# Performance work log

Hardware: AMD Instinct MI355X
Metric: run time of the kernel (lower is better)

The kernel has to match this reference:

```python
import jax, jax.numpy as jnp
import numpy as np

N_TOPICS = 1024
TOPIC_DIM = 128
HIDDEN = 512
N_HEADS = 8
HEAD_DIM = HIDDEN // N_HEADS
N_LAYERS = 2
ALPHA = 0.2
TIME_DECAY = 0.1
BATCH = 8


def setup_inputs() -> dict:
    key = jax.random.key(0)
    ks = jax.random.split(key, 16)
    inp = {
        'topic_ids': jax.random.randint(ks[0], (BATCH,), 0, N_TOPICS, dtype=jnp.int32),
        'adj_matrix': jax.random.randint(ks[1], (BATCH, N_TOPICS, N_TOPICS), 0, 2, dtype=jnp.int32),
        'time_matrix': jax.random.uniform(ks[2], (BATCH, N_TOPICS, N_TOPICS), dtype=jnp.float32),
        'attractiveness': jax.random.normal(ks[3], (BATCH,), dtype=jnp.float32),
        # parameters (torch Linear convention: W [out,in], y = x@W.T + b)
        'topic_embedding': jax.random.normal(ks[4], (N_TOPICS, TOPIC_DIM), dtype=jnp.float32) * 0.1,
        'struct_W': jax.random.normal(ks[5], (HIDDEN, TOPIC_DIM), dtype=jnp.float32) * 0.05,
        'struct_b': jnp.zeros((HIDDEN,), dtype=jnp.float32),
        'attract_W': jax.random.normal(ks[6], (HIDDEN, 1), dtype=jnp.float32) * 0.05,
        'attract_b': jnp.zeros((HIDDEN,), dtype=jnp.float32),
        'gat_W': jax.random.normal(ks[7], (N_LAYERS, N_HEADS, HIDDEN, HEAD_DIM), dtype=jnp.float32) * 0.05,
        'gat_a': jax.random.normal(ks[8], (N_LAYERS, N_HEADS, 2 * HEAD_DIM, 1), dtype=jnp.float32) * 0.05,
        'fc1_W': jax.random.normal(ks[9], (HIDDEN, HIDDEN), dtype=jnp.float32) * 0.05,
        'fc1_b': jnp.zeros((HIDDEN,), dtype=jnp.float32),
        'fc2_W': jax.random.normal(ks[10], (1, HIDDEN), dtype=jnp.float32) * 0.05,
        'fc2_b': jnp.zeros((1,), dtype=jnp.float32),
    }
    return inp


def _gat_layer(node, adj, time_w, W, a):
    # node: [B,N,F], adj: [B,N,N] (0/1), time_w: [B,N,N]
    # W: [H,F,hd], a: [H,2*hd,1]
    h = jnp.einsum('bni,hio->bhno', node, W)  # [B,H,N,hd]
    # Additive attention: a = [a_src; a_dst] so e_ij = LeakyReLU(h_i.a_src + h_j.a_dst)
    a_src = a[:, :HEAD_DIM, 0]   # [H,hd]
    a_dst = a[:, HEAD_DIM:, 0]   # [H,hd]
    e_src = jnp.einsum('bhnd,hd->bhn', h, a_src)  # [B,H,N]
    e_dst = jnp.einsum('bhnd,hd->bhn', h, a_dst)  # [B,H,N]
    e = e_src[:, :, :, None] + e_dst[:, :, None, :]  # [B,H,N,N]
    e = jax.nn.leaky_relu(e, negative_slope=ALPHA)
    e = e * time_w[:, None, :, :]
    e = jnp.where(adj[:, None, :, :] == 0, -jnp.inf, e)
    attn = jax.nn.softmax(e, axis=-1)
    out = jnp.einsum('bhij,bhjd->bhid', attn, h)  # [B,H,N,hd]
    out = out.transpose(0, 2, 1, 3).reshape(node.shape[0], node.shape[1], -1)
    return jax.nn.elu(out)


def reference(topic_ids, adj_matrix, time_matrix, attractiveness,
              topic_embedding, struct_W, struct_b, attract_W, attract_b,
              gat_W, gat_a, fc1_W, fc1_b, fc2_W, fc2_b):
    # structural features for all topics -> hidden
    struct = topic_embedding @ struct_W.T + struct_b          # [N,hidden]
    attract = attractiveness[:, None] @ attract_W.T + attract_b  # [B,hidden]
    node = jnp.broadcast_to(struct[None], (BATCH, N_TOPICS, HIDDEN))
    # weighted co-occurrence time (eq.17)
    time_w = jnp.exp(-TIME_DECAY * (time_matrix.max() - time_matrix))  # [B,N,N]
    for l in range(N_LAYERS):
        node = _gat_layer(node, adj_matrix, time_w, gat_W[l], gat_a[l])
    # gather per-sample topic node feature
    topic_feat = jnp.take_along_axis(node, topic_ids[:, None, None].astype(jnp.int32), axis=1)[:, 0]  # [B,hidden]
    combined = topic_feat + attract
    hidden = jax.nn.relu(combined @ fc1_W.T + fc1_b)
    pred = hidden @ fc2_W.T + fc2_b  # [B,1]
    return pred
```

## Files before the change

kernel.cpp:

```cpp
#include <hip/hip_runtime.h>

#define NT 1024
#define TD 128
#define HID 512
#define NH 8
#define HD 64
#define NB 8

typedef unsigned short us;
typedef _Float16 h16;
typedef h16 half8 __attribute__((ext_vector_type(8)));
typedef h16 h16x2 __attribute__((ext_vector_type(2)));
typedef float f32x4 __attribute__((ext_vector_type(4)));

#define LOG2E 1.44269504f

extern "C" __device__ _Float16 __ocml_exp2_f16(_Float16);

__device__ __forceinline__ us f2h(float x) { return __builtin_bit_cast(us, (h16)x); }
__device__ __forceinline__ float h2f(us s) { return (float)__builtin_bit_cast(h16, s); }
__device__ __forceinline__ unsigned int pkh2(float a, float b) {
    auto v = __builtin_amdgcn_cvt_pkrtz(a, b);
    return __builtin_bit_cast(unsigned int, v);
}

__global__ __launch_bounds__(256) void kprep(const float* __restrict__ tm, float* __restrict__ part,
                                             const float* __restrict__ emb, const float* __restrict__ sW,
                                             const float* __restrict__ sb, us* __restrict__ node0b,
                                             const float* __restrict__ gW, us* __restrict__ Wt,
                                             const float* __restrict__ fc2b, float* __restrict__ out) {
    __shared__ __align__(16) float smf[8768];
    int bx = blockIdx.x, t = threadIdx.x;
    if (bx < 1024) {
        const float4* tm4 = (const float4*)tm;
        size_t base = (size_t)bx * 256 + t;
        float m = -1e30f;
        #pragma unroll
        for (int k = 0; k < 8; k++) {
            float4 v = tm4[base + (size_t)k * 262144];
            m = fmaxf(m, fmaxf(fmaxf(v.x, v.y), fmaxf(v.z, v.w)));
        }
        smf[t] = m; __syncthreads();
        for (int s = 128; s > 0; s >>= 1) { if (t < s) smf[t] = fmaxf(smf[t], smf[t + s]); __syncthreads(); }
        if (t == 0) part[bx] = smf[0];
    } else if (bx < 1152) {
        int g = bx - 1024; int iblk = g & 15, oseg = g >> 4;
        us* As = (us*)smf;
        us* Bs = (us*)smf + 64 * 136;
        const float4* esrc = (const float4*)(emb + (size_t)iblk * 64 * TD);
        const float4* wsrc = (const float4*)(sW + (size_t)oseg * 64 * TD);
        #pragma unroll
        for (int rep = 0; rep < 8; rep++) {
            int f = rep * 256 + t;
            int row = f >> 5, c4 = f & 31;
            float4 av = esrc[f];
            float4 bv = wsrc[f];
            uint2 pa, pb;
            pa.x = pkh2(av.x, av.y); pa.y = pkh2(av.z, av.w);
            pb.x = pkh2(bv.x, bv.y); pb.y = pkh2(bv.z, bv.w);
            *(uint2*)&As[row * 136 + c4 * 4] = pa;
            *(uint2*)&Bs[row * 136 + c4 * 4] = pb;
        }
        __syncthreads();
        int l = t & 63, w = t >> 6, m = l & 15, q = l >> 4;
        f32x4 acc[4];
        #pragma unroll
        for (int ot = 0; ot < 4; ot++) acc[ot] = (f32x4){0.f, 0.f, 0.f, 0.f};
        #pragma unroll
        for (int ks = 0; ks < 4; ks++) {
            half8 a = *(const half8*)&As[(w * 16 + m) * 136 + ks * 32 + q * 8];
            #pragma unroll
            for (int ot = 0; ot < 4; ot++) {
                half8 b = *(const half8*)&Bs[(ot * 16 + m) * 136 + ks * 32 + q * 8];
                acc[ot] = __builtin_amdgcn_mfma_f32_16x16x32_f16(a, b, acc[ot], 0, 0, 0);
            }
        }
        #pragma unroll
        for (int ot = 0; ot < 4; ot++) {
            int col = oseg * 64 + ot * 16 + m;
            float sbv = sb[col];
            #pragma unroll
            for (int rr = 0; rr < 4; rr++) {
                int rowi = iblk * 64 + w * 16 + q * 4 + rr;
                node0b[(size_t)rowi * HID + col] = f2h(acc[ot][rr] + sbv);
            }
        }
    } else {
        int g = bx - 1152; int lh = g >> 3, kt = g & 7;
        if (g == 0 && t < NB) out[t] = fc2b[0];
        float* tile = smf;
        const float4* src = (const float4*)(gW + ((size_t)lh * HID + kt * 64) * HD);
        #pragma unroll
        for (int rep = 0; rep < 4; rep++) {
            int f = rep * 256 + t;
            float4 v = src[f];
            int row = f >> 4, col = (f & 15) * 4;
            float* d = tile + row * 65 + col;
            d[0] = v.x; d[1] = v.y; d[2] = v.z; d[3] = v.w;
        }
        __syncthreads();
        int o = t >> 2, ks = (t & 3) * 16;
        us pk[16];
        #pragma unroll
        for (int j = 0; j < 16; j++) pk[j] = f2h(tile[(ks + j) * 65 + o]);
        us* dst = Wt + (size_t)lh * HD * HID + (size_t)o * HID + kt * 64 + ks;
        *(uint4*)dst = *(uint4*)pk;
        *(uint4*)(dst + 8) = *(uint4*)&pk[8];
    }
}

__device__ __forceinline__ void gemm_body(const us* __restrict__ A, const us* __restrict__ W,
                                          const float* __restrict__ gav,
                                          us* __restrict__ outT, us* __restrict__ outR,
                                          float* __restrict__ esO, float* __restrict__ edO,
                                          int iblk, int b, int h, int t, us* sm) {
    us* As = sm;
    us* Bs = sm + 2 * 4608;
    int row = t >> 2, ks = t & 3;
    int l = t & 63, w = t >> 6, m = l & 15, q = l >> 4;
    size_t arow0 = (size_t)(b * NT + iblk * 64);
    const us* ar = A + (arow0 + row) * HID + ks * 16;
    const us* br = W + ((size_t)(h * HD + row)) * HID + ks * 16;
    f32x4 acc[4];
    #pragma unroll
    for (int ot = 0; ot < 4; ot++) acc[ot] = (f32x4){0.f, 0.f, 0.f, 0.f};
    {
        uint4 x0 = *(const uint4*)ar, x1 = *(const uint4*)(ar + 8);
        uint4 y0 = *(const uint4*)br, y1 = *(const uint4*)(br + 8);
        *(uint4*)&As[row * 72 + ks * 16] = x0; *(uint4*)&As[row * 72 + ks * 16 + 8] = x1;
        *(uint4*)&Bs[row * 72 + ks * 16] = y0; *(uint4*)&Bs[row * 72 + ks * 16 + 8] = y1;
    }
    uint4 a0 = *(const uint4*)(ar + 64), a1 = *(const uint4*)(ar + 72);
    uint4 b0 = *(const uint4*)(br + 64), b1 = *(const uint4*)(br + 72);
    for (int it = 0; it < 8; it++) {
        int cur = it & 1, nxt = cur ^ 1;
        uint4 na0, na1, nb0, nb1;
        if (it < 6) {
            int k0 = (it + 2) * 64;
            na0 = *(const uint4*)(ar + k0); na1 = *(const uint4*)(ar + k0 + 8);
            nb0 = *(const uint4*)(br + k0); nb1 = *(const uint4*)(br + k0 + 8);
        }
        __syncthreads();
        if (it < 7) {
            *(uint4*)&As[nxt * 4608 + row * 72 + ks * 16] = a0;
            *(uint4*)&As[nxt * 4608 + row * 72 + ks * 16 + 8] = a1;
            *(uint4*)&Bs[nxt * 4608 + row * 72 + ks * 16] = b0;
            *(uint4*)&Bs[nxt * 4608 + row * 72 + ks * 16 + 8] = b1;
        }
        const us* Ac = As + cur * 4608; const us* Bc = Bs + cur * 4608;
        #pragma unroll
        for (int kt = 0; kt < 2; kt++) {
            half8 av = *(const half8*)&Ac[(w * 16 + m) * 72 + kt * 32 + q * 8];
            #pragma unroll
            for (int ot = 0; ot < 4; ot++) {
                half8 bv = *(const half8*)&Bc[(ot * 16 + m) * 72 + kt * 32 + q * 8];
                acc[ot] = __builtin_amdgcn_mfma_f32_16x16x32_f16(av, bv, acc[ot], 0, 0, 0);
            }
        }
        if (it < 6) { a0 = na0; a1 = na1; b0 = nb0; b1 = nb1; }
    }
    const float* gas = gav + h * 2 * HD;
    float gs[4], gd[4];
    #pragma unroll
    for (int ot = 0; ot < 4; ot++) { gs[ot] = gas[ot * 16 + m]; gd[ot] = gas[HD + ot * 16 + m]; }
    size_t ebase = ((size_t)b * NH + h) * NT + iblk * 64;
    #pragma unroll
    for (int rr = 0; rr < 4; rr++) {
        float s = 0.f, d = 0.f;
        #pragma unroll
        for (int ot = 0; ot < 4; ot++) { float v = acc[ot][rr]; s = fmaf(v, gs[ot], s); d = fmaf(v, gd[ot], d); }
        #pragma unroll
        for (int mask = 1; mask < 16; mask <<= 1) { s += __shfl_xor(s, mask); d += __shfl_xor(d, mask); }
        if (m == 0) {
            int rowi = w * 16 + q * 4 + rr;
            esO[ebase + rowi] = s;
            edO[ebase + rowi] = d;
        }
    }
    #pragma unroll
    for (int ot = 0; ot < 4; ot++) {
        int col = h * HD + ot * 16 + m;
        #pragma unroll
        for (int rr = 0; rr < 4; rr++) {
            int i_loc = w * 16 + q * 4 + rr;
            float v = acc[ot][rr];
            if (outT) outT[(size_t)col * NT + iblk * 64 + i_loc] = f2h(v);
            if (outR) outR[(arow0 + i_loc) * HID + col] = f2h(v);
        }
    }
}

__global__ __launch_bounds__(256) void kphase1(const float* __restrict__ tm, const int* __restrict__ adj,
                                               const float* __restrict__ part, us* __restrict__ TWb,
                                               const us* __restrict__ node0b, const us* __restrict__ Wt,
                                               const float* __restrict__ ga, us* __restrict__ Ht1,
                                               float* __restrict__ es1, float* __restrict__ ed1) {
    __shared__ __align__(16) us sm[4 * 4608];
    int bx = blockIdx.x, t = threadIdx.x;
    if (bx < 2048) {
        float* red = (float*)sm;
        float m = fmaxf(fmaxf(part[t * 4], part[t * 4 + 1]), fmaxf(part[t * 4 + 2], part[t * 4 + 3]));
        red[t] = m; __syncthreads();
        for (int s = 128; s > 0; s >>= 1) { if (t < s) red[t] = fmaxf(red[t], red[t + s]); __syncthreads(); }
        float tmx = red[0];
        const float C = 0.1f * LOG2E;
        const float NANF = __uint_as_float(0x7FC00000u);
        #pragma unroll
        for (int it = 0; it < 4; it++) {
            size_t idx = (((size_t)bx * 4 + it) * 256 + t) * 4;
            float4 tv = *(const float4*)(tm + idx);
            int4 av = *(const int4*)(adj + idx);
            float w0 = exp2f((tv.x - tmx) * C) * LOG2E;
            float w1 = exp2f((tv.y - tmx) * C) * LOG2E;
            float w2 = exp2f((tv.z - tmx) * C) * LOG2E;
            float w3 = exp2f((tv.w - tmx) * C) * LOG2E;
            w0 = av.x ? w0 : NANF;
            w1 = av.y ? w1 : NANF;
            w2 = av.z ? w2 : NANF;
            w3 = av.w ? w3 : NANF;
            uint2 pk;
            pk.x = pkh2(w0, w1);
            pk.y = pkh2(w2, w3);
            *(uint2*)&TWb[idx] = pk;
        }
    } else {
        int g = bx - 2048;
        gemm_body(node0b, Wt, ga, Ht1, nullptr, es1, ed1, g & 15, 0, g >> 4, t, sm);
    }
}

__global__ __launch_bounds__(256) void kgemm2(const us* __restrict__ node1b, const us* __restrict__ Wt2,
                                              const float* __restrict__ ga2, us* __restrict__ H2b,
                                              float* __restrict__ es2, float* __restrict__ ed2) {
    __shared__ __align__(16) us sm[4 * 4608];
    int n = blockIdx.x;
    int b = n & 7, k = n >> 3, iblk = k & 15, h = k >> 4;
    gemm_body(node1b, Wt2, ga2, nullptr, H2b, es2, ed2, iblk, b, h, threadIdx.x, sm);
}

__device__ __forceinline__ unsigned int p_word_fly(unsigned int tw, unsigned int ed, h16x2 es) {
    h16x2 t = __builtin_bit_cast(h16x2, tw);
    h16x2 d = __builtin_bit_cast(h16x2, ed);
    h16x2 e = es + d;
    h16x2 lk = e * (h16)0.2f;
    h16x2 el = __builtin_elementwise_max(e, lk);
    h16x2 mm = t * el;
    h16x2 p;
    p.x = __ocml_exp2_f16(mm.x);
    p.y = __ocml_exp2_f16(mm.y);
    h16x2 z = {(h16)0.0f, (h16)0.0f};
    h16x2 r = __builtin_elementwise_max(p, z);
    return __builtin_bit_cast(unsigned int, r);
}

__device__ __forceinline__ void compute_p_fly(uint4 T0, uint4 T1, uint4 D0, uint4 D1, h16x2 es,
                                              uint4& P01, uint4& P23) {
    P01.x = p_word_fly(T0.x, D0.x, es);
    P01.y = p_word_fly(T0.y, D0.y, es);
    P01.z = p_word_fly(T0.z, D0.z, es);
    P01.w = p_word_fly(T0.w, D0.w, es);
    P23.x = p_word_fly(T1.x, D1.x, es);
    P23.y = p_word_fly(T1.y, D1.y, es);
    P23.z = p_word_fly(T1.z, D1.z, es);
    P23.w = p_word_fly(T1.w, D1.w, es);
}

__global__ __launch_bounds__(256) void kattn1(const us* __restrict__ TWb, const us* __restrict__ Ht,
                                              const float* __restrict__ es1, const float* __restrict__ ed1,
                                              us* __restrict__ node1b) {
    int n = blockIdx.x;
    int b = n & 7, k = n >> 3, iblk = k & 15, h = k >> 4;
    int t = threadIdx.x;
    __shared__ __align__(16) us Ps[2 * 4608];
    __shared__ __align__(16) us Hs[2 * 4608];
    __shared__ __align__(16) us edl[NT];
    __shared__ float invl_s[64];
    int i = t >> 2, js = t & 3;
    int l = t & 63, w = t >> 6, m = l & 15, q = l >> 4;
    {
        float4 ev = *(const float4*)&ed1[h * NT + t * 4];
        uint2 pk; pk.x = pkh2(ev.x, ev.y); pk.y = pkh2(ev.z, ev.w);
        *(uint2*)&edl[t * 4] = pk;
    }
    float esf = es1[h * NT + iblk * 64 + i];
    h16 esh = (h16)esf;
    h16x2 esv = {esh, esh};
    const us* twrow = TWb + ((size_t)(b * NT) + iblk * 64 + i) * NT + js * 16;
    const us* htrow = Ht + ((size_t)(h * HD) + i) * NT + js * 16;
    f32x4 acc[4];
    #pragma unroll
    for (int ot = 0; ot < 4; ot++) acc[ot] = (f32x4){0.f, 0.f, 0.f, 0.f};
    f32x4 acc1 = (f32x4){0.f, 0.f, 0.f, 0.f};
    h16 ov = (m == 0) ? (h16)1.0f : (h16)0.0f;
    half8 bones = {ov, ov, ov, ov, ov, ov, ov, ov};
    uint4 T0, T1, Hh0, Hh1;
    T0 = *(const uint4*)twrow; T1 = *(const uint4*)(twrow + 8);
    Hh0 = *(const uint4*)htrow; Hh1 = *(const uint4*)(htrow + 8);
    __syncthreads();
    {
        uint4 D0 = *(const uint4*)&edl[js * 16];
        uint4 D1 = *(const uint4*)&edl[js * 16 + 8];
        uint4 p01, p23;
        compute_p_fly(T0, T1, D0, D1, esv, p01, p23);
        us* Pd = Ps + i * 72 + js * 16;
        us* Hd = Hs + i * 72 + js * 16;
        *(uint4*)Pd = p01; *(uint4*)(Pd + 8) = p23;
        *(uint4*)Hd = Hh0; *(uint4*)(Hd + 8) = Hh1;
    }
    T0 = *(const uint4*)(twrow + 64); T1 = *(const uint4*)(twrow + 72);
    Hh0 = *(const uint4*)(htrow + 64); Hh1 = *(const uint4*)(htrow + 72);
    for (int it = 0; it < 16; it++) {
        int cur = it & 1, nxt = cur ^ 1;
        uint4 nT0, nT1, nH0, nH1;
        if (it < 14) {
            int j0 = (it + 2) * 64;
            nT0 = *(const uint4*)(twrow + j0); nT1 = *(const uint4*)(twrow + j0 + 8);
            nH0 = *(const uint4*)(htrow + j0); nH1 = *(const uint4*)(htrow + j0 + 8);
        }
        uint4 p01, p23;
        if (it < 15) {
            int j0 = (it + 1) * 64;
            uint4 D0 = *(const uint4*)&edl[j0 + js * 16];
            uint4 D1 = *(const uint4*)&edl[j0 + js * 16 + 8];
            compute_p_fly(T0, T1, D0, D1, esv, p01, p23);
        }
        __syncthreads();
        if (it < 15) {
            us* Pd = Ps + nxt * 4608 + i * 72 + js * 16;
            us* Hd = Hs + nxt * 4608 + i * 72 + js * 16;
            *(uint4*)Pd = p01; *(uint4*)(Pd + 8) = p23;
            *(uint4*)Hd = Hh0; *(uint4*)(Hd + 8) = Hh1;
        }
        const us* Pc = Ps + cur * 4608; const us* Hc = Hs + cur * 4608;
        #pragma unroll
        for (int kt = 0; kt < 2; kt++) {
            half8 av = *(const half8*)&Pc[(w * 16 + m) * 72 + kt * 32 + q * 8];
            #pragma unroll
            for (int ot = 0; ot < 4; ot++) {
                half8 bv = *(const half8*)&Hc[(ot * 16 + m) * 72 + kt * 32 + q * 8];
                acc[ot] = __builtin_amdgcn_mfma_f32_16x16x32_f16(av, bv, acc[ot], 0, 0, 0);
            }
            acc1 = __builtin_amdgcn_mfma_f32_16x16x32_f16(av, bones, acc1, 0, 0, 0);
        }
        if (it < 14) { T0 = nT0; T1 = nT1; Hh0 = nH0; Hh1 = nH1; }
    }
    if (m == 0) {
        #pragma unroll
        for (int rr = 0; rr < 4; rr++) invl_s[w * 16 + q * 4 + rr] = 1.f / acc1[rr];
    }
    __syncthreads();
    #pragma unroll
    for (int ot = 0; ot < 4; ot++) {
        int col = h * HD + ot * 16 + m;
        #pragma unroll
        for (int rr = 0; rr < 4; rr++) {
            int i_loc = w * 16 + q * 4 + rr;
            float v = acc[ot][rr] * invl_s[i_loc];
            v = v > 0.f ? v : (__expf(v) - 1.f);
            node1b[(size_t)(b * NT + iblk * 64 + i_loc) * HID + col] = f2h(v);
        }
    }
}

__global__ __launch_bounds__(256) void kattn2a(const us* __restrict__ TWb, const us* __restrict__ H2b,
                                               const float* __restrict__ es2, const float* __restrict__ ed2,
                                               const int* __restrict__ topic_ids,
                                               float* __restrict__ ppv, float* __restrict__ pl) {
    int js = blockIdx.x, h = blockIdx.y, b = blockIdx.z;
    int t = threadIdx.x;
    __shared__ float pls[64];
    __shared__ float red[256];
    int qi = topic_ids[b];
    if (t < 64) {
        int j = js * 64 + t;
        float esq = es2[((size_t)b * NH + h) * NT + qi];
        float tw = h2f(TWb[((size_t)(b * NT) + qi) * NT + j]);
        float e = esq + ed2[((size_t)b * NH + h) * NT + j];
        e = fmaxf(e, 0.2f * e) * tw;
        float p = fmaxf(exp2f(e), 0.f);
        pls[t] = p;
        float lsum = p;
        #pragma unroll
        for (int mask = 1; mask < 64; mask <<= 1) lsum += __shfl_xor(lsum, mask);
        if (t == 0) pl[((size_t)b * NH + h) * 16 + js] = lsum;
    }
    __syncthreads();
    int o = t & 63, jg = t >> 6;
    float acc = 0.f;
    const us* hb = H2b + ((size_t)(b * NT) + js * 64 + jg * 16) * HID + h * HD + o;
    #pragma unroll
    for (int jj = 0; jj < 16; jj++)
        acc = fmaf(pls[jg * 16 + jj], h2f(hb[(size_t)jj * HID]), acc);
    red[t] = acc; __syncthreads();
    if (t < 64) {
        float pv = red[t] + red[t + 64] + red[t + 128] + red[t + 192];
        ppv[(((size_t)b * NH + h) * 16 + js) * HD + t] = pv;
    }
}

__global__ __launch_bounds__(256) void khead2(const float* __restrict__ ppv, const float* __restrict__ pl,
                                              const float* __restrict__ attr,
                                              const float* __restrict__ aW, const float* __restrict__ ab,
                                              const float* __restrict__ fc1W, const float* __restrict__ fc1b,
                                              const float* __restrict__ fc2W, float* __restrict__ out) {
    int kseg = blockIdx.x, b = blockIdx.y;
    int t = threadIdx.x;
    __shared__ float comb[HID];
    __shared__ float linv[NH];
    __shared__ float r2[256];
    if (t < NH) {
        float lsum = 0.f;
        #pragma unroll
        for (int js = 0; js < 16; js++) lsum += pl[((size_t)b * NH + t) * 16 + js];
        linv[t] = 1.f / lsum;
    }
    __syncthreads();
    float av = attr[b];
    for (int k = t; k < HID; k += 256) {
        int h = k >> 6, o = k & 63;
        float pv = 0.f;
        #pragma unroll
        for (int js = 0; js < 16; js++) pv += ppv[(((size_t)b * NH + h) * 16 + js) * HD + o];
        float v = pv * linv[h];
        v = v > 0.f ? v : (__expf(v) - 1.f);
        comb[k] = v + av * aW[k] + ab[k];
    }
    __syncthreads();
    int kk = kseg * 16 + (t >> 4);
    int j = t & 15;
    const float* row = fc1W + (size_t)kk * HID;
    float acc = 0.f;
    #pragma unroll 8
    for (int mi = 0; mi < 32; mi++) {
        int idx = mi * 16 + j;
        acc = fmaf(comb[idx], row[idx], acc);
    }
    #pragma unroll
    for (int mask = 1; mask < 16; mask <<= 1) acc += __shfl_xor(acc, mask);
    float partv = 0.f;
    if (j == 0) {
        float hk = fmaxf(acc + fc1b[kk], 0.f);
        partv = hk * fc2W[kk];
    }
    r2[t] = partv; __syncthreads();
    for (int s = 128; s > 0; s >>= 1) { if (t < s) r2[t] += r2[t + s]; __syncthreads(); }
    if (t == 0) atomicAdd(&out[b], r2[0]);
}

extern "C" void kernel_launch(void* const* d_in, const int* in_sizes, int n_in,
                              void* d_out, int out_size, void* d_ws, size_t ws_size,
                              hipStream_t stream) {
    const int*   topic_ids = (const int*)d_in[0];
    const int*   adj       = (const int*)d_in[1];
    const float* tm        = (const float*)d_in[2];
    const float* attr      = (const float*)d_in[3];
    const float* emb       = (const float*)d_in[4];
    const float* sW        = (const float*)d_in[5];
    const float* sb        = (const float*)d_in[6];
    const float* aW        = (const float*)d_in[7];
    const float* ab        = (const float*)d_in[8];
    const float* gW        = (const float*)d_in[9];
    const float* ga        = (const float*)d_in[10];
    const float* fc1W      = (const float*)d_in[11];
    const float* fc1b      = (const float*)d_in[12];
    const float* fc2W      = (const float*)d_in[13];
    const float* fc2b      = (const float*)d_in[14];
    float* out = (float*)d_out;

    char* p = (char*)d_ws;
    us* TWb    = (us*)p; p += sizeof(us) * (size_t)NB * NT * NT;
    us* node0b = (us*)p; p += sizeof(us) * (size_t)NT * HID;
    us* Wt     = (us*)p; p += sizeof(us) * (size_t)2 * NH * HD * HID;
    us* Ht1    = (us*)p; p += sizeof(us) * (size_t)HID * NT;
    us* node1b = (us*)p; p += sizeof(us) * (size_t)NB * NT * HID;
    us* H2b    = (us*)p; p += sizeof(us) * (size_t)NB * NT * HID;
    float* es1  = (float*)p; p += sizeof(float) * NH * NT;
    float* ed1  = (float*)p; p += sizeof(float) * NH * NT;
    float* es2  = (float*)p; p += sizeof(float) * NB * NH * NT;
    float* ed2  = (float*)p; p += sizeof(float) * NB * NH * NT;
    float* ppv  = (float*)p; p += sizeof(float) * NB * NH * 16 * HD;
    float* pl   = (float*)p; p += sizeof(float) * NB * NH * 16;
    float* part = (float*)p; p += sizeof(float) * 1024;

    kprep<<<1280, 256, 0, stream>>>(tm, part, emb, sW, sb, node0b, gW, Wt, fc2b, out);
    kphase1<<<2176, 256, 0, stream>>>(tm, adj, part, TWb, node0b, Wt, ga, Ht1, es1, ed1);
    kattn1<<<1024, 256, 0, stream>>>(TWb, Ht1, es1, ed1, node1b);
    kgemm2<<<1024, 256, 0, stream>>>(node1b, Wt + (size_t)NH * HD * HID,
                                     ga + NH * 2 * HD, H2b, es2, ed2);
    kattn2a<<<dim3(16, NH, NB), 256, 0, stream>>>(TWb, H2b, es2, ed2, topic_ids, ppv, pl);
    khead2<<<dim3(32, NB), 256, 0, stream>>>(ppv, pl, attr, aW, ab, fc1W, fc1b, fc2W, out);
}
```

Baseline: 187.9 us.

## Compute attention P fragments directly in registers and double rows per block

The layer-1 attention kernel now gives each block 128 query rows instead of 64, halving the grid to 512 blocks so each staged H tile in shared memory is reused across twice as many rows. The probability fragments are computed straight into MFMA operand registers from per-lane time-weight loads, which removes the shared-memory staging buffer for P and its reads. The cost is more accumulator registers per thread, possibly lower occupancy, and fewer blocks to cover the GPU.

```diff
diff --git a/kernel.cpp b/kernel.cpp
--- a/kernel.cpp
+++ b/kernel.cpp
@@ -253,111 +253,115 @@
     return __builtin_bit_cast(unsigned int, r);
 }
 
-__device__ __forceinline__ void compute_p_fly(uint4 T0, uint4 T1, uint4 D0, uint4 D1, h16x2 es,
-                                              uint4& P01, uint4& P23) {
-    P01.x = p_word_fly(T0.x, D0.x, es);
-    P01.y = p_word_fly(T0.y, D0.y, es);
-    P01.z = p_word_fly(T0.z, D0.z, es);
-    P01.w = p_word_fly(T0.w, D0.w, es);
-    P23.x = p_word_fly(T1.x, D1.x, es);
-    P23.y = p_word_fly(T1.y, D1.y, es);
-    P23.z = p_word_fly(T1.z, D1.z, es);
-    P23.w = p_word_fly(T1.w, D1.w, es);
+__device__ __forceinline__ half8 p_frag(uint4 T, uint4 D, h16x2 es) {
+    uint4 r;
+    r.x = p_word_fly(T.x, D.x, es);
+    r.y = p_word_fly(T.y, D.y, es);
+    r.z = p_word_fly(T.z, D.z, es);
+    r.w = p_word_fly(T.w, D.w, es);
+    return __builtin_bit_cast(half8, r);
 }
 
 __global__ __launch_bounds__(256) void kattn1(const us* __restrict__ TWb, const us* __restrict__ Ht,
                                               const float* __restrict__ es1, const float* __restrict__ ed1,
                                               us* __restrict__ node1b) {
     int n = blockIdx.x;
-    int b = n & 7, k = n >> 3, iblk = k & 15, h = k >> 4;
+    int b = n & 7, k = n >> 3;
+    int i2 = k & 7, h = k >> 3;
     int t = threadIdx.x;
-    __shared__ __align__(16) us Ps[2 * 4608];
-    __shared__ __align__(16) us Hs[2 * 4608];
+    __shared__ __align__(16) us Hs[2][64 * 72];
     __shared__ __align__(16) us edl[NT];
-    __shared__ float invl_s[64];
-    int i = t >> 2, js = t & 3;
+    __shared__ float invl_s[128];
     int l = t & 63, w = t >> 6, m = l & 15, q = l >> 4;
     {
         float4 ev = *(const float4*)&ed1[h * NT + t * 4];
         uint2 pk; pk.x = pkh2(ev.x, ev.y); pk.y = pkh2(ev.z, ev.w);
         *(uint2*)&edl[t * 4] = pk;
     }
-    float esf = es1[h * NT + iblk * 64 + i];
-    h16 esh = (h16)esf;
-    h16x2 esv = {esh, esh};
-    const us* twrow = TWb + ((size_t)(b * NT) + iblk * 64 + i) * NT + js * 16;
-    const us* htrow = Ht + ((size_t)(h * HD) + i) * NT + js * 16;
-    f32x4 acc[4];
-    #pragma unroll
-    for (int ot = 0; ot < 4; ot++) acc[ot] = (f32x4){0.f, 0.f, 0.f, 0.f};
-    f32x4 acc1 = (f32x4){0.f, 0.f, 0.f, 0.f};
+    int rowA = i2 * 128 + w * 32 + m;
+    h16 eA = (h16)es1[h * NT + rowA];
+    h16 eB = (h16)es1[h * NT + rowA + 16];
+    h16x2 esvA = {eA, eA}, esvB = {eB, eB};
+    const us* twA = TWb + ((size_t)(b * NT) + rowA) * NT + q * 8;
+    const us* twB = twA + (size_t)16 * NT;
+    int hr = t >> 2, js = t & 3;
+    const us* htrow = Ht + ((size_t)(h * HD) + hr) * NT + js * 16;
+    f32x4 acc[2][4];
+    #pragma unroll
+    for (int ti = 0; ti < 2; ti++)
+        #pragma unroll
+        for (int ot = 0; ot < 4; ot++) acc[ti][ot] = (f32x4){0.f, 0.f, 0.f, 0.f};
+    f32x4 acc1[2] = {(f32x4){0.f, 0.f, 0.f, 0.f}, (f32x4){0.f, 0.f, 0.f, 0.f}};
     h16 ov = (m == 0) ? (h16)1.0f : (h16)0.0f;
     half8 bones = {ov, ov, ov, ov, ov, ov, ov, ov};
-    uint4 T0, T1, Hh0, Hh1;
-    T0 = *(const uint4*)twrow; T1 = *(const uint4*)(twrow + 8);
-    Hh0 = *(const uint4*)htrow; Hh1 = *(const uint4*)(htrow + 8);
+    uint4 H0 = *(const uint4*)htrow, H1 = *(const uint4*)(htrow + 8);
+    *(uint4*)&Hs[0][hr * 72 + js * 16] = H0;
+    *(uint4*)&Hs[0][hr * 72 + js * 16 + 8] = H1;
+    H0 = *(const uint4*)(htrow + 64); H1 = *(const uint4*)(htrow + 72);
+    uint4 TA0 = *(const uint4*)twA,        TA1 = *(const uint4*)(twA + 32);
+    uint4 TB0 = *(const uint4*)twB,        TB1 = *(const uint4*)(twB + 32);
     __syncthreads();
-    {
-        uint4 D0 = *(const uint4*)&edl[js * 16];
-        uint4 D1 = *(const uint4*)&edl[js * 16 + 8];
-        uint4 p01, p23;
-        compute_p_fly(T0, T1, D0, D1, esv, p01, p23);
-        us* Pd = Ps + i * 72 + js * 16;
-        us* Hd = Hs + i * 72 + js * 16;
-        *(uint4*)Pd = p01; *(uint4*)(Pd + 8) = p23;
-        *(uint4*)Hd = Hh0; *(uint4*)(Hd + 8) = Hh1;
-    }
-    T0 = *(const uint4*)(twrow + 64); T1 = *(const uint4*)(twrow + 72);
-    Hh0 = *(const uint4*)(htrow + 64); Hh1 = *(const uint4*)(htrow + 72);
     for (int it = 0; it < 16; it++) {
         int cur = it & 1, nxt = cur ^ 1;
-        uint4 nT0, nT1, nH0, nH1;
+        int j0 = it * 64;
+        uint4 nH0, nH1, nA0, nA1, nB0, nB1;
         if (it < 14) {
-            int j0 = (it + 2) * 64;
-            nT0 = *(const uint4*)(twrow + j0); nT1 = *(const uint4*)(twrow + j0 + 8);
-            nH0 = *(const uint4*)(htrow + j0); nH1 = *(const uint4*)(htrow + j0 + 8);
-        }
-        uint4 p01, p23;
+            nH0 = *(const uint4*)(htrow + j0 + 128);
+            nH1 = *(const uint4*)(htrow + j0 + 136);
+        }
         if (it < 15) {
-            int j0 = (it + 1) * 64;
-            uint4 D0 = *(const uint4*)&edl[j0 + js * 16];
-            uint4 D1 = *(const uint4*)&edl[j0 + js * 16 + 8];
-            compute_p_fly(T0, T1, D0, D1, esv, p01, p23);
-        }
+            nA0 = *(const uint4*)(twA + j0 + 64);  nA1 = *(const uint4*)(twA + j0 + 96);
+            nB0 = *(const uint4*)(twB + j0 + 64);  nB1 = *(const uint4*)(twB + j0 + 96);
+        }
+        uint4 D0 = *(const uint4*)&edl[j0 + q * 8];
+        uint4 D1 = *(const uint4*)&edl[j0 + 32 + q * 8];
+        half8 pA0 = p_frag(TA0, D0, esvA);
+        half8 pA1 = p_frag(TA1, D1, esvA);
+        half8 pB0 = p_frag(TB0, D0, esvB);
+        half8 pB1 = p_frag(TB1, D1, esvB);
         __syncthreads();
         if (it < 15) {
-            us* Pd = Ps + nxt * 4608 + i * 72 + js * 16;
-            us* Hd = Hs + nxt * 4608 + i * 72 + js * 16;
-            *(uint4*)Pd = p01; *(uint4*)(Pd + 8) = p23;
-            *(uint4*)Hd = Hh0; *(uint4*)(Hd + 8) = Hh1;
-        }
-        const us* Pc = Ps + cur * 4608; const us* Hc = Hs + cur * 4608;
-        #pragma unroll
-        for (int kt = 0; kt < 2; kt++) {
-            half8 av = *(const half8*)&Pc[(w * 16 + m) * 72 + kt * 32 + q * 8];
+            *(uint4*)&Hs[nxt][hr * 72 + js * 16] = H0;
+            *(uint4*)&Hs[nxt][hr * 72 + js * 16 + 8] = H1;
+        }
+        const us* Hc = Hs[cur];
+        #pragma unroll
+        for (int ot = 0; ot < 4; ot++) {
+            half8 bv0 = *(const half8*)&Hc[(ot * 16 + m) * 72 + q * 8];
+            half8 bv1 = *(const half8*)&Hc[(ot * 16 + m) * 72 + 32 + q * 8];
+            acc[0][ot] = __builtin_amdgcn_mfma_f32_16x16x32_f16(pA0, bv0, acc[0][ot], 0, 0, 0);
+            acc[0][ot] = __builtin_amdgcn_mfma_f32_16x16x32_f16(pA1, bv1, acc[0][ot], 0, 0, 0);
+            acc[1][ot] = __builtin_amdgcn_mfma_f32_16x16x32_f16(pB0, bv0, acc[1][ot], 0, 0, 0);
+            acc[1][ot] = __builtin_amdgcn_mfma_f32_16x16x32_f16(pB1, bv1, acc[1][ot], 0, 0, 0);
+        }
+        acc1[0] = __builtin_amdgcn_mfma_f32_16x16x32_f16(pA0, bones, acc1[0], 0, 0, 0);
+        acc1[0] = __builtin_amdgcn_mfma_f32_16x16x32_f16(pA1, bones, acc1[0], 0, 0, 0);
+        acc1[1] = __builtin_amdgcn_mfma_f32_16x16x32_f16(pB0, bones, acc1[1], 0, 0, 0);
+        acc1[1] = __builtin_amdgcn_mfma_f32_16x16x32_f16(pB1, bones, acc1[1], 0, 0, 0);
+        if (it < 14) { H0 = nH0; H1 = nH1; }
+        if (it < 15) { TA0 = nA0; TA1 = nA1; TB0 = nB0; TB1 = nB1; }
+    }
+    if (m == 0) {
+        #pragma unroll
+        for (int rr = 0; rr < 4; rr++) {
+            invl_s[w * 32 + q * 4 + rr]      = 1.f / acc1[0][rr];
+            invl_s[w * 32 + 16 + q * 4 + rr] = 1.f / acc1[1][rr];
+        }
+    }
+    __syncthreads();
+    size_t rbase = (size_t)(b * NT + i2 * 128);
+    #pragma unroll
+    for (int ti = 0; ti < 2; ti++) {
+        #pragma unroll
+        for (int ot = 0; ot < 4; ot++) {
+            int col = h * HD + ot * 16 + m;
             #pragma unroll
-            for (int ot = 0; ot < 4; ot++) {
-                half8 bv = *(const half8*)&Hc[(ot * 16 + m) * 72 + kt * 32 + q * 8];
-                acc[ot] = __builtin_amdgcn_mfma_f32_16x16x32_f16(av, bv, acc[ot], 0, 0, 0);
+            for (int rr = 0; rr < 4; rr++) {
+                int rloc = w * 32 + ti * 16 + q * 4 + rr;
+                float v = acc[ti][ot][rr] * invl_s[rloc];
+                v = v > 0.f ? v : (__expf(v) - 1.f);
+                node1b[(rbase + rloc) * HID + col] = f2h(v);
             }
-            acc1 = __builtin_amdgcn_mfma_f32_16x16x32_f16(av, bones, acc1, 0, 0, 0);
-        }
-        if (it < 14) { T0 = nT0; T1 = nT1; Hh0 = nH0; Hh1 = nH1; }
-    }
-    if (m == 0) {
-        #pragma unroll
-        for (int rr = 0; rr < 4; rr++) invl_s[w * 16 + q * 4 + rr] = 1.f / acc1[rr];
-    }
-    __syncthreads();
-    #pragma unroll
-    for (int ot = 0; ot < 4; ot++) {
-        int col = h * HD + ot * 16 + m;
-        #pragma unroll
-        for (int rr = 0; rr < 4; rr++) {
-            int i_loc = w * 16 + q * 4 + rr;
-            float v = acc[ot][rr] * invl_s[i_loc];
-            v = v > 0.f ? v : (__expf(v) - 1.f);
-            node1b[(size_t)(b * NT + iblk * 64 + i_loc) * HID + col] = f2h(v);
         }
     }
 }
@@ -484,7 +488,7 @@
 
     kprep<<<1280, 256, 0, stream>>>(tm, part, emb, sW, sb, node0b, gW, Wt, fc2b, out);
     kphase1<<<2176, 256, 0, stream>>>(tm, adj, part, TWb, node0b, Wt, ga, Ht1, es1, ed1);
-    kattn1<<<1024, 256, 0, stream>>>(TWb, Ht1, es1, ed1, node1b);
+    kattn1<<<512, 256, 0, stream>>>(TWb, Ht1, es1, ed1, node1b);
     kgemm2<<<1024, 256, 0, stream>>>(node1b, Wt + (size_t)NH * HD * HID,
                                      ga + NH * 2 * HD, H2b, es2, ed2);
     kattn2a<<<dim3(16, NH, NB), 256, 0, stream>>>(TWb, H2b, es2, ed2, topic_ids, ppv, pl);
```

New measurement: 186.9 us. No clear change (-0.5%).
